# Kernel optimization log

Measured on AMD Instinct MI355X. Metric: run time of the kernel, lower is better.

## Reference

```python
import jax, jax.numpy as jnp
import numpy as np

UNITS = 512
INPUT_DIM = 64
BATCH = 131072


def setup_inputs() -> dict:
    key = jax.random.key(0)
    kx, kw = jax.random.split(key)
    x = jax.random.normal(kx, (BATCH, INPUT_DIM), dtype=jnp.float32)
    w = jax.random.normal(kw, (UNITS, INPUT_DIM), dtype=jnp.float32) * 0.05
    return {"x": x, "w": w}


def reference(x, w):
    # Pairwise squared L2 distance: dist[b, u] = sum_d (w[u,d] - x[b,d])^2
    # avoids the O(B*U*D) broadcast intermediate).
    x_sq = jnp.sum(x * x, axis=-1, keepdims=True)        # [B, 1]
    w_sq = jnp.sum(w * w, axis=-1)[None, :]              # [1, U]
    cross = jnp.einsum("bd,ud->bu", x, w)                # [B, U]
    return x_sq + w_sq - 2.0 * cross
```

## Files before the change

kernel.cpp:

```cpp
#include <hip/hip_runtime.h>

#define BATCH 131072
#define UNITS 512
#define DIM   64
#define BM    128

typedef __attribute__((ext_vector_type(8))) short  short8;
typedef __attribute__((ext_vector_type(4))) float  floatx4;

static __device__ __forceinline__ unsigned short f32_to_bf16(float f) {
    union { float f; unsigned int u; } c; c.f = f;
    unsigned int u = c.u;
    unsigned int r = u + 0x7fffu + ((u >> 16) & 1u);
    return (unsigned short)(r >> 16);
}

__global__ __launch_bounds__(256) void prep_w_kernel(
    const float* __restrict__ w,
    unsigned short* __restrict__ wb,
    float* __restrict__ wsq)
{
    const int u = blockIdx.x * 4 + (threadIdx.x >> 6);
    const int d = threadIdx.x & 63;
    float v = w[u * DIM + d];
    wb[u * DIM + d] = f32_to_bf16(v);
    float s = v * v;
    #pragma unroll
    for (int o = 32; o > 0; o >>= 1) s += __shfl_xor(s, o);
    if (d == 0) wsq[u] = s;
}

__global__ __launch_bounds__(256) void dist_kernel(
    const float* __restrict__ x,
    const unsigned short* __restrict__ wb,
    const float* __restrict__ wsq,
    float* __restrict__ out)
{
    __shared__ __align__(16) float wsq_s[UNITS];

    const int tid  = threadIdx.x;
    const int row0 = blockIdx.x * BM;

    wsq_s[tid]       = wsq[tid];
    wsq_s[tid + 256] = wsq[tid + 256];
    __syncthreads();

    const int wave = tid >> 6;
    const int lane = tid & 63;
    const int l15  = lane & 15;
    const int quad = lane >> 4;
    const int mrow = wave * 32;

    short8 a[2][2];
    float  xs2[2];
    #pragma unroll
    for (int mf = 0; mf < 2; ++mf) {
        const float* xr = x + (size_t)(row0 + mrow + mf * 16 + l15) * DIM;
        float v[16];
        *(float4*)&v[0]  = *(const float4*)(xr + quad * 8);
        *(float4*)&v[4]  = *(const float4*)(xr + quad * 8 + 4);
        *(float4*)&v[8]  = *(const float4*)(xr + 32 + quad * 8);
        *(float4*)&v[12] = *(const float4*)(xr + 32 + quad * 8 + 4);
        float s = 0.f;
        unsigned short p[16];
        #pragma unroll
        for (int i = 0; i < 16; ++i) { s += v[i] * v[i]; p[i] = f32_to_bf16(v[i]); }
        a[mf][0] = *(short8*)&p[0];
        a[mf][1] = *(short8*)&p[8];
        s += __shfl_xor(s, 16);
        s += __shfl_xor(s, 32);
        xs2[mf] = s;
    }

    const short8* wv = (const short8*)wb;

    for (int gu = 0; gu < 8; ++gu) {
        const int colb = gu * 64;

        short8  b[4][2];
        floatx4 wq[4];
        #pragma unroll
        for (int t = 0; t < 4; ++t) {
            const short8* bp = wv + (size_t)(colb + t * 16 + l15) * 8;
            b[t][0] = bp[quad];
            b[t][1] = bp[quad + 4];
            wq[t]   = *(const floatx4*)&wsq_s[colb + t * 16 + quad * 4];
        }

        #pragma unroll
        for (int mf = 0; mf < 2; ++mf) {
            #pragma unroll
            for (int t = 0; t < 4; ++t) {
                floatx4 acc = floatx4{0.f, 0.f, 0.f, 0.f};
                acc = __builtin_amdgcn_mfma_f32_16x16x32_bf16(b[t][0], a[mf][0], acc, 0, 0, 0);
                acc = __builtin_amdgcn_mfma_f32_16x16x32_bf16(b[t][1], a[mf][1], acc, 0, 0, 0);

                floatx4 vo;
                #pragma unroll
                for (int i = 0; i < 4; ++i)
                    vo[i] = xs2[mf] + wq[t][i] - 2.0f * acc[i];

                float* dst = out + (size_t)(row0 + mrow + mf * 16 + l15) * UNITS
                                 + colb + t * 16 + quad * 4;
                __builtin_nontemporal_store(vo, (floatx4*)dst);
            }
        }
    }
}

extern "C" void kernel_launch(void* const* d_in, const int* in_sizes, int n_in,
                              void* d_out, int out_size, void* d_ws, size_t ws_size,
                              hipStream_t stream) {
    const float* x = (const float*)d_in[0];
    const float* w = (const float*)d_in[1];
    float* out = (float*)d_out;

    unsigned short* wb  = (unsigned short*)d_ws;
    float*          wsq = (float*)((char*)d_ws + UNITS * DIM * 2);

    prep_w_kernel<<<UNITS / 4, 256, 0, stream>>>(w, wb, wsq);
    dist_kernel<<<BATCH / BM, 256, 0, stream>>>(x, wb, wsq, out);
}
```

Before: 328.4 us.

## Stage output tile in LDS for coalesced full-row stores with smaller row blocks

Shrinks the row block to 16 rows and splits the 512 columns across the four waves. Each wave writes its MFMA results into a padded shared-memory tile. After a barrier, each wave streams whole 2 KB output rows with contiguous 16-byte nontemporal stores, replacing the previous scattered 64-byte segments per row. The block count rises eightfold and the W fragments are reloaded per block. This adds about 33 KB of LDS per block and an extra barrier, with an occupancy hint of 4 blocks per CU.

New measurement: 330.2 us. About the same (+0.6%).

```diff
diff --git a/kernel.cpp b/kernel.cpp
--- a/kernel.cpp
+++ b/kernel.cpp
@@ -3,7 +3,8 @@
 #define BATCH 131072
 #define UNITS 512
 #define DIM   64
-#define BM    128
+#define BM    16
+#define STF   516
 
 typedef __attribute__((ext_vector_type(8))) short  short8;
 typedef __attribute__((ext_vector_type(4))) float  floatx4;
@@ -30,32 +31,30 @@
     if (d == 0) wsq[u] = s;
 }
 
-__global__ __launch_bounds__(256) void dist_kernel(
+__global__ __launch_bounds__(256, 4) void dist_kernel(
     const float* __restrict__ x,
     const unsigned short* __restrict__ wb,
     const float* __restrict__ wsq,
     float* __restrict__ out)
 {
-    __shared__ __align__(16) float wsq_s[UNITS];
+    __shared__ float wsq_s[UNITS];
+    __shared__ __align__(16) float st[BM][STF];
 
     const int tid  = threadIdx.x;
     const int row0 = blockIdx.x * BM;
 
     wsq_s[tid]       = wsq[tid];
     wsq_s[tid + 256] = wsq[tid + 256];
-    __syncthreads();
 
     const int wave = tid >> 6;
     const int lane = tid & 63;
     const int l15  = lane & 15;
     const int quad = lane >> 4;
-    const int mrow = wave * 32;
 
-    short8 a[2][2];
-    float  xs2[2];
-    #pragma unroll
-    for (int mf = 0; mf < 2; ++mf) {
-        const float* xr = x + (size_t)(row0 + mrow + mf * 16 + l15) * DIM;
+    short8 a[2];
+    float  xs;
+    {
+        const float* xr = x + (size_t)(row0 + l15) * DIM;
         float v[16];
         *(float4*)&v[0]  = *(const float4*)(xr + quad * 8);
         *(float4*)&v[4]  = *(const float4*)(xr + quad * 8 + 4);
@@ -65,45 +64,58 @@
         unsigned short p[16];
         #pragma unroll
         for (int i = 0; i < 16; ++i) { s += v[i] * v[i]; p[i] = f32_to_bf16(v[i]); }
-        a[mf][0] = *(short8*)&p[0];
-        a[mf][1] = *(short8*)&p[8];
+        a[0] = *(short8*)&p[0];
+        a[1] = *(short8*)&p[8];
         s += __shfl_xor(s, 16);
         s += __shfl_xor(s, 32);
-        xs2[mf] = s;
+        xs = s;
     }
+    float xsm[4];
+    #pragma unroll
+    for (int i = 0; i < 4; ++i) xsm[i] = __shfl(xs, quad * 4 + i);
+
+    __syncthreads();
 
     const short8* wv = (const short8*)wb;
 
-    for (int gu = 0; gu < 8; ++gu) {
-        const int colb = gu * 64;
+    #pragma unroll
+    for (int g = 0; g < 2; ++g) {
+        const int colb = (wave * 2 + g) * 64;
 
-        short8  b[4][2];
-        floatx4 wq[4];
+        short8 b2[4][2];
+        float  wq[4];
         #pragma unroll
         for (int t = 0; t < 4; ++t) {
             const short8* bp = wv + (size_t)(colb + t * 16 + l15) * 8;
-            b[t][0] = bp[quad];
-            b[t][1] = bp[quad + 4];
-            wq[t]   = *(const floatx4*)&wsq_s[colb + t * 16 + quad * 4];
+            b2[t][0] = bp[quad];
+            b2[t][1] = bp[quad + 4];
+            wq[t]    = wsq_s[colb + t * 16 + l15];
         }
 
         #pragma unroll
-        for (int mf = 0; mf < 2; ++mf) {
+        for (int t = 0; t < 4; ++t) {
+            floatx4 acc = floatx4{0.f, 0.f, 0.f, 0.f};
+            acc = __builtin_amdgcn_mfma_f32_16x16x32_bf16(a[0], b2[t][0], acc, 0, 0, 0);
+            acc = __builtin_amdgcn_mfma_f32_16x16x32_bf16(a[1], b2[t][1], acc, 0, 0, 0);
+
             #pragma unroll
-            for (int t = 0; t < 4; ++t) {
-                floatx4 acc = floatx4{0.f, 0.f, 0.f, 0.f};
-                acc = __builtin_amdgcn_mfma_f32_16x16x32_bf16(b[t][0], a[mf][0], acc, 0, 0, 0);
-                acc = __builtin_amdgcn_mfma_f32_16x16x32_bf16(b[t][1], a[mf][1], acc, 0, 0, 0);
+            for (int i = 0; i < 4; ++i)
+                st[quad * 4 + i][colb + t * 16 + l15] =
+                    xsm[i] + wq[t] - 2.0f * acc[i];
+        }
+    }
 
-                floatx4 vo;
-                #pragma unroll
-                for (int i = 0; i < 4; ++i)
-                    vo[i] = xs2[mf] + wq[t][i] - 2.0f * acc[i];
+    __syncthreads();
 
-                float* dst = out + (size_t)(row0 + mrow + mf * 16 + l15) * UNITS
-                                 + colb + t * 16 + quad * 4;
-                __builtin_nontemporal_store(vo, (floatx4*)dst);
-            }
+    #pragma unroll
+    for (int j = 0; j < 4; ++j) {
+        const int r = wave * 4 + j;
+        const float* src = &st[r][0];
+        float* dst = out + (size_t)(row0 + r) * UNITS;
+        #pragma unroll
+        for (int h = 0; h < 2; ++h) {
+            const floatx4 vv = *(const floatx4*)(src + h * 256 + lane * 4);
+            __builtin_nontemporal_store(vv, (floatx4*)(dst + h * 256 + lane * 4));
         }
     }
 }
```

## Stage pre-swizzled bf16 W fragments in LDS and process two row tiles per block

Applied to the files above, without the earlier changes.

A new prep kernel writes W in MFMA-fragment order, and each block copies all 64 KB of it into shared memory once, then reads B fragments from LDS instead of strided global loads. Each block now handles two 128-row tiles with all A fragments loaded up front, and uses launch bounds of 2 blocks per CU. Output stores switch from nontemporal to regular stores. The aim is to cut repeated global/L2 traffic for W. The cost is a large LDS footprint that limits occupancy, plus an extra kernel launch, and regular stores may pollute cache on this store-bound workload.

Result: faster. 313.0 us (-4.7%).

```diff
diff --git a/kernel.cpp b/kernel.cpp
--- a/kernel.cpp
+++ b/kernel.cpp
@@ -4,6 +4,8 @@
 #define UNITS 512
 #define DIM   64
 #define BM    128
+#define TILES 2
+#define NFRAG 4096
 
 typedef __attribute__((ext_vector_type(8))) short  short8;
 typedef __attribute__((ext_vector_type(4))) float  floatx4;
@@ -15,94 +17,120 @@
     return (unsigned short)(r >> 16);
 }
 
-__global__ __launch_bounds__(256) void prep_w_kernel(
-    const float* __restrict__ w,
-    unsigned short* __restrict__ wb,
-    float* __restrict__ wsq)
+__global__ __launch_bounds__(256) void prep_wsq_kernel(
+    const float* __restrict__ w, float* __restrict__ wsq)
 {
     const int u = blockIdx.x * 4 + (threadIdx.x >> 6);
     const int d = threadIdx.x & 63;
     float v = w[u * DIM + d];
-    wb[u * DIM + d] = f32_to_bf16(v);
     float s = v * v;
     #pragma unroll
     for (int o = 32; o > 0; o >>= 1) s += __shfl_xor(s, o);
     if (d == 0) wsq[u] = s;
 }
 
-__global__ __launch_bounds__(256) void dist_kernel(
+__global__ __launch_bounds__(256) void prep_wfrag_kernel(
+    const float* __restrict__ w, uint4* __restrict__ wbf)
+{
+    const int tid  = blockIdx.x * 256 + threadIdx.x;
+    const int lane = tid & 63;
+    const int fi   = tid >> 6;
+    const int h    = fi & 1;
+    const int tt   = fi >> 1;
+    const int u    = (tt >> 2) * 64 + (tt & 3) * 16 + (lane & 15);
+    const int k0   = h * 32 + (lane >> 4) * 8;
+    const float* src = w + u * DIM + k0;
+    float v[8];
+    *(float4*)&v[0] = *(const float4*)src;
+    *(float4*)&v[4] = *(const float4*)(src + 4);
+    unsigned short p[8];
+    #pragma unroll
+    for (int i = 0; i < 8; ++i) p[i] = f32_to_bf16(v[i]);
+    wbf[tid] = *(uint4*)p;
+}
+
+__global__ __launch_bounds__(256, 2) void dist_kernel(
     const float* __restrict__ x,
-    const unsigned short* __restrict__ wb,
+    const uint4* __restrict__ wbf,
     const float* __restrict__ wsq,
     float* __restrict__ out)
 {
+    __shared__ __align__(16) uint4 wbs[NFRAG];
     __shared__ __align__(16) float wsq_s[UNITS];
 
     const int tid  = threadIdx.x;
-    const int row0 = blockIdx.x * BM;
-
-    wsq_s[tid]       = wsq[tid];
-    wsq_s[tid + 256] = wsq[tid + 256];
-    __syncthreads();
-
     const int wave = tid >> 6;
     const int lane = tid & 63;
     const int l15  = lane & 15;
     const int quad = lane >> 4;
     const int mrow = wave * 32;
+    const int row0 = blockIdx.x * (BM * TILES);
 
-    short8 a[2][2];
-    float  xs2[2];
+    #pragma unroll 4
+    for (int i = 0; i < 16; ++i)
+        wbs[i * 256 + tid] = wbf[i * 256 + tid];
+    wsq_s[tid]       = wsq[tid];
+    wsq_s[tid + 256] = wsq[tid + 256];
+
+    short8 a[TILES][2][2];
+    float  xs2[TILES][2];
     #pragma unroll
-    for (int mf = 0; mf < 2; ++mf) {
-        const float* xr = x + (size_t)(row0 + mrow + mf * 16 + l15) * DIM;
-        float v[16];
-        *(float4*)&v[0]  = *(const float4*)(xr + quad * 8);
-        *(float4*)&v[4]  = *(const float4*)(xr + quad * 8 + 4);
-        *(float4*)&v[8]  = *(const float4*)(xr + 32 + quad * 8);
-        *(float4*)&v[12] = *(const float4*)(xr + 32 + quad * 8 + 4);
-        float s = 0.f;
-        unsigned short p[16];
-        #pragma unroll
-        for (int i = 0; i < 16; ++i) { s += v[i] * v[i]; p[i] = f32_to_bf16(v[i]); }
-        a[mf][0] = *(short8*)&p[0];
-        a[mf][1] = *(short8*)&p[8];
-        s += __shfl_xor(s, 16);
-        s += __shfl_xor(s, 32);
-        xs2[mf] = s;
-    }
-
-    const short8* wv = (const short8*)wb;
-
-    for (int gu = 0; gu < 8; ++gu) {
-        const int colb = gu * 64;
-
-        short8  b[4][2];
-        floatx4 wq[4];
-        #pragma unroll
-        for (int t = 0; t < 4; ++t) {
-            const short8* bp = wv + (size_t)(colb + t * 16 + l15) * 8;
-            b[t][0] = bp[quad];
-            b[t][1] = bp[quad + 4];
-            wq[t]   = *(const floatx4*)&wsq_s[colb + t * 16 + quad * 4];
-        }
-
+    for (int tl = 0; tl < TILES; ++tl) {
         #pragma unroll
         for (int mf = 0; mf < 2; ++mf) {
+            const float* xr = x + (size_t)(row0 + tl * BM + mrow + mf * 16 + l15) * DIM;
+            float v[16];
+            *(float4*)&v[0]  = *(const float4*)(xr + quad * 8);
+            *(float4*)&v[4]  = *(const float4*)(xr + quad * 8 + 4);
+            *(float4*)&v[8]  = *(const float4*)(xr + 32 + quad * 8);
+            *(float4*)&v[12] = *(const float4*)(xr + 32 + quad * 8 + 4);
+            float s = 0.f;
+            unsigned short p[16];
+            #pragma unroll
+            for (int i = 0; i < 16; ++i) { s += v[i] * v[i]; p[i] = f32_to_bf16(v[i]); }
+            a[tl][mf][0] = *(short8*)&p[0];
+            a[tl][mf][1] = *(short8*)&p[8];
+            s += __shfl_xor(s, 16);
+            s += __shfl_xor(s, 32);
+            xs2[tl][mf] = s;
+        }
+    }
+    __syncthreads();
+
+    #pragma unroll
+    for (int tl = 0; tl < TILES; ++tl) {
+        for (int gu = 0; gu < 8; ++gu) {
+            const int colb = gu * 64;
+
+            short8  b[4][2];
+            floatx4 wq[4];
             #pragma unroll
             for (int t = 0; t < 4; ++t) {
-                floatx4 acc = floatx4{0.f, 0.f, 0.f, 0.f};
-                acc = __builtin_amdgcn_mfma_f32_16x16x32_bf16(b[t][0], a[mf][0], acc, 0, 0, 0);
-                acc = __builtin_amdgcn_mfma_f32_16x16x32_bf16(b[t][1], a[mf][1], acc, 0, 0, 0);
+                const int fb = ((gu * 4 + t) * 2) * 64 + lane;
+                uint4 r0 = wbs[fb];
+                uint4 r1 = wbs[fb + 64];
+                b[t][0] = *(short8*)&r0;
+                b[t][1] = *(short8*)&r1;
+                wq[t]   = *(const floatx4*)&wsq_s[colb + t * 16 + quad * 4];
+            }
 
-                floatx4 vo;
+            #pragma unroll
+            for (int mf = 0; mf < 2; ++mf) {
                 #pragma unroll
-                for (int i = 0; i < 4; ++i)
-                    vo[i] = xs2[mf] + wq[t][i] - 2.0f * acc[i];
+                for (int t = 0; t < 4; ++t) {
+                    floatx4 acc = floatx4{0.f, 0.f, 0.f, 0.f};
+                    acc = __builtin_amdgcn_mfma_f32_16x16x32_bf16(b[t][0], a[tl][mf][0], acc, 0, 0, 0);
+                    acc = __builtin_amdgcn_mfma_f32_16x16x32_bf16(b[t][1], a[tl][mf][1], acc, 0, 0, 0);
 
-                float* dst = out + (size_t)(row0 + mrow + mf * 16 + l15) * UNITS
-                                 + colb + t * 16 + quad * 4;
-                __builtin_nontemporal_store(vo, (floatx4*)dst);
+                    floatx4 vo;
+                    #pragma unroll
+                    for (int i = 0; i < 4; ++i)
+                        vo[i] = xs2[tl][mf] + wq[t][i] - 2.0f * acc[i];
+
+                    float* dst = out + (size_t)(row0 + tl * BM + mrow + mf * 16 + l15) * UNITS
+                                     + colb + t * 16 + quad * 4;
+                    *(floatx4*)dst = vo;
+                }
             }
         }
     }
@@ -115,9 +143,10 @@
     const float* w = (const float*)d_in[1];
     float* out = (float*)d_out;
 
-    unsigned short* wb  = (unsigned short*)d_ws;
-    float*          wsq = (float*)((char*)d_ws + UNITS * DIM * 2);
+    uint4* wbf = (uint4*)d_ws;
+    float* wsq = (float*)((char*)d_ws + NFRAG * sizeof(uint4));
 
-    prep_w_kernel<<<UNITS / 4, 256, 0, stream>>>(w, wb, wsq);
-    dist_kernel<<<BATCH / BM, 256, 0, stream>>>(x, wb, wsq, out);
+    prep_wsq_kernel<<<UNITS / 4, 256, 0, stream>>>(w, wsq);
+    prep_wfrag_kernel<<<NFRAG / 256, 256, 0, stream>>>(w, wbf);
+    dist_kernel<<<BATCH / (BM * TILES), 256, 0, stream>>>(x, wbf, wsq, out);
 }
```
